# Optimization experiments

Hardware: AMD Instinct MI355X
Metric: run time of the kernel (lower is better)

The kernel has to match this reference:

```python
import jax, jax.numpy as jnp
import numpy as np

NUM_HEADS = 8
WIN = 8

def setup_inputs() -> dict:
    key = jax.random.key(0)
    k1, k2, k3 = jax.random.split(key, 3)
    B, H, W, C = 4, 256, 256, 256
    x = jax.random.normal(k1, (B, H, W, C), dtype=jnp.float32)
    w_qkv = jax.random.normal(k2, (C, 3 * C), dtype=jnp.float32) * (1.0 / np.sqrt(C))
    b_qkv = jnp.zeros((3 * C,), dtype=jnp.float32)
    w_proj = jax.random.normal(k3, (C, C), dtype=jnp.float32) * (1.0 / np.sqrt(C))
    b_proj = jnp.zeros((C,), dtype=jnp.float32)
    return {"x": x, "w_qkv": w_qkv, "b_qkv": b_qkv, "w_proj": w_proj, "b_proj": b_proj}

def reference(x, w_qkv, b_qkv, w_proj, b_proj):
    B, H, W, C = x.shape
    ws = WIN
    pad_h = (ws - H % ws) % ws
    pad_w = (ws - W % ws) % ws
    if pad_h > 0 or pad_w > 0:
        x = jnp.pad(x, ((0, 0), (0, pad_h), (0, pad_w), (0, 0)), mode='reflect')
        H, W = H + pad_h, W + pad_w
    Ho, Wo = H - pad_h, W - pad_w
    # window partition: [B, H//ws, ws, W//ws, ws, C] -> [nW, ws*ws, C]
    xw = x.reshape(B, H // ws, ws, W // ws, ws, C)
    xw = xw.transpose(0, 1, 3, 2, 4, 5).reshape(-1, ws * ws, C)
    head_dim = C // NUM_HEADS
    scale = head_dim ** (-0.5)
    qkv = xw @ w_qkv + b_qkv  # [nW, T, 3C]
    qkv = qkv.reshape(-1, ws * ws, 3, NUM_HEADS, head_dim).transpose(2, 0, 3, 1, 4)
    q, k, v = qkv[0], qkv[1], qkv[2]  # each [nW, h, T, d]
    attn = jnp.einsum('whtd,whsd->whts', q, k) * scale
    attn = jax.nn.softmax(attn, axis=-1)
    o = jnp.einsum('whts,whsd->whtd', attn, v)
    o = o.transpose(0, 2, 1, 3).reshape(-1, ws * ws, C)
    o = o @ w_proj + b_proj
    # window merge
    o = o.reshape(B, H // ws, W // ws, ws, ws, C)
    o = o.transpose(0, 1, 3, 2, 4, 5).reshape(B, H, W, C)
    return o[:, :Ho, :Wo, :]
```

## Files before the change

### kernel.cpp

```cpp
#include <hip/hip_runtime.h>
#include <hip/hip_bf16.h>

typedef __attribute__((ext_vector_type(8))) short short8;
typedef __attribute__((ext_vector_type(4))) short short4v;
typedef __attribute__((ext_vector_type(4))) float f32x4;

#define MFMA(a, b, c) __builtin_amdgcn_mfma_f32_16x16x32_bf16(a, b, c, 0, 0, 0)
#define XS(t, c) (((t) << 8) + ((c) ^ (((t) & 7) << 3)))

__device__ __forceinline__ unsigned int pk2(float lo, float hi) {
    union { __hip_bfloat162 h2; unsigned int u; } cv;
    cv.h2 = __float22bfloat162_rn(make_float2(lo, hi));
    return cv.u;
}

__device__ __forceinline__ unsigned short f2bf1(float f) {
    unsigned int u = __float_as_uint(f);
    u += 0x7FFFu + ((u >> 16) & 1u);
    return (unsigned short)(u >> 16);
}

__device__ __forceinline__ short4v u2s4(uint2 p) {
    union { uint2 u; short4v s; } t; t.u = p; return t.s;
}

#if __has_builtin(__builtin_amdgcn_mfma_f32_16x16x16bf16_1k)
__device__ __forceinline__ f32x4 mfma16(uint2 a, uint2 b, f32x4 c) {
    return __builtin_amdgcn_mfma_f32_16x16x16bf16_1k(u2s4(a), u2s4(b), c, 0, 0, 0);
}
#else
__device__ __forceinline__ short8 zfrag(uint2 p) {
    union { unsigned int u[4]; short8 s; } t;
    t.u[0] = p.x; t.u[1] = p.y; t.u[2] = 0u; t.u[3] = 0u;
    return t.s;
}
__device__ __forceinline__ f32x4 mfma16(uint2 a, uint2 b, f32x4 c) {
    return MFMA(zfrag(a), zfrag(b), c);
}
#endif

#define EXP2(x) exp2f(x)

__global__ void prep_w(const float* __restrict__ wqkv, const float* __restrict__ wproj,
                       unsigned short* __restrict__ wT) {
    int idx = blockIdx.x * 256 + threadIdx.x;
    if (idx < 196608) {
        const int frag   = idx >> 9;
        const int within = idx & 511;
        const int lane = within >> 3, j = within & 7;
        const int ks = frag & 7;
        const int dt = (frag >> 3) & 1;
        const int hh = (frag >> 4) & 7;
        const int m  = frag >> 7;
        const int n = m * 256 + hh * 32 + dt * 16 + (lane & 15);
        const int k = ks * 32 + ((lane >> 4) << 3) + j;
        wT[idx] = f2bf1(wqkv[k * 768 + n]);
    } else {
        const int r = idx - 196608;
        const int n = r >> 8, k = r & 255;
        wT[idx] = f2bf1(wproj[(k << 8) + n]);
    }
}

__global__ __launch_bounds__(256, 2)
void attn_qkv(const float* __restrict__ x,
              const float* __restrict__ bqkv,
              const unsigned short* __restrict__ wpk,
              unsigned short* __restrict__ Ob)
{
    __shared__ unsigned short smem[64 * 256];

    const int tid  = threadIdx.x;
    const int wid  = tid >> 6;
    const int lane = tid & 63;
    const int g    = lane >> 4;
    const int q16  = lane & 15;

    const int bid  = blockIdx.x;
    const int xcd  = bid & 7;
    const int q    = bid >> 3;
    const int widx = xcd * 512 + (q >> 1);
    const int hq   = (q & 1) << 2;
    const int h    = hq + wid;

    const int b  = widx >> 10;
    const int wh = (widx >> 5) & 31;
    const int ww = widx & 31;

    {
        const int t  = tid >> 2;
        const int c0 = (tid & 3) << 3;
        const int hr = (wh << 3) + (t >> 3);
        const int wc = (ww << 3) + (t & 7);
        const float* rowp = x + (((size_t)b * 256 + hr) * 256 + wc) * 256;
        #pragma unroll
        for (int u = 0; u < 8; ++u) {
            const int c = c0 + (u << 5);
            const float4 f0 = *reinterpret_cast<const float4*>(rowp + c);
            const float4 f1 = *reinterpret_cast<const float4*>(rowp + c + 4);
            union { unsigned int u4[4]; short8 s; } pv;
            pv.u4[0] = pk2(f0.x, f0.y); pv.u4[1] = pk2(f0.z, f0.w);
            pv.u4[2] = pk2(f1.x, f1.y); pv.u4[3] = pk2(f1.z, f1.w);
            *reinterpret_cast<short8*>(&smem[XS(t, c)]) = pv.s;
        }
    }
    __syncthreads();

    const f32x4 fz = {0.f, 0.f, 0.f, 0.f};
    const float SCL = 0.17677669529663687f * 1.4426950408889634f;
    const unsigned short* wh0 = wpk + ((size_t)h << 13);
    const int loff = lane << 3;

    uint2 pq[2][4];
    {
        f32x4 acc[2][4];
        #pragma unroll
        for (int dt = 0; dt < 2; ++dt)
            #pragma unroll
            for (int tt = 0; tt < 4; ++tt) acc[dt][tt] = fz;
        #pragma unroll
        for (int ks = 0; ks < 8; ++ks) {
            const int kc = ks << 5;
            short8 xf[4];
            #pragma unroll
            for (int tt = 0; tt < 4; ++tt)
                xf[tt] = *reinterpret_cast<const short8*>(&smem[XS(tt * 16 + q16, kc + (g << 3))]);
            #pragma unroll
            for (int dt = 0; dt < 2; ++dt) {
                const short8 wf = *reinterpret_cast<const short8*>(
                    wh0 + (((dt << 3) + ks) << 9) + loff);
                #pragma unroll
                for (int tt = 0; tt < 4; ++tt)
                    acc[dt][tt] = MFMA(wf, xf[tt], acc[dt][tt]);
            }
        }
        #pragma unroll
        for (int dt = 0; dt < 2; ++dt) {
            const float4 bb = *reinterpret_cast<const float4*>(bqkv + h * 32 + dt * 16 + (g << 2));
            #pragma unroll
            for (int tt = 0; tt < 4; ++tt) {
                const f32x4 a = acc[dt][tt];
                pq[dt][tt] = make_uint2(pk2((a[0] + bb.x) * SCL, (a[1] + bb.y) * SCL),
                                        pk2((a[2] + bb.z) * SCL, (a[3] + bb.w) * SCL));
            }
        }
    }

    uint2 pkk[2][4];
    {
        f32x4 acc[2][4];
        #pragma unroll
        for (int dt = 0; dt < 2; ++dt)
            #pragma unroll
            for (int tt = 0; tt < 4; ++tt) acc[dt][tt] = fz;
        const unsigned short* wb = wh0 + ((size_t)8 << 13);
        #pragma unroll
        for (int ks = 0; ks < 8; ++ks) {
            const int kc = ks << 5;
            short8 xf[4];
            #pragma unroll
            for (int tt = 0; tt < 4; ++tt)
                xf[tt] = *reinterpret_cast<const short8*>(&smem[XS(tt * 16 + q16, kc + (g << 3))]);
            #pragma unroll
            for (int dt = 0; dt < 2; ++dt) {
                const short8 wf = *reinterpret_cast<const short8*>(
                    wb + (((dt << 3) + ks) << 9) + loff);
                #pragma unroll
                for (int tt = 0; tt < 4; ++tt)
                    acc[dt][tt] = MFMA(wf, xf[tt], acc[dt][tt]);
            }
        }
        #pragma unroll
        for (int dt = 0; dt < 2; ++dt) {
            const float4 bb = *reinterpret_cast<const float4*>(bqkv + 256 + h * 32 + dt * 16 + (g << 2));
            #pragma unroll
            for (int tt = 0; tt < 4; ++tt) {
                const f32x4 a = acc[dt][tt];
                pkk[dt][tt] = make_uint2(pk2(a[0] + bb.x, a[1] + bb.y),
                                         pk2(a[2] + bb.z, a[3] + bb.w));
            }
        }
    }

    uint2 ppk[4][4];
    float inv4[4];
    #pragma unroll
    for (int qt = 0; qt < 4; ++qt) {
        f32x4 st[4];
        #pragma unroll
        for (int kt = 0; kt < 4; ++kt) st[kt] = fz;
        #pragma unroll
        for (int dt = 0; dt < 2; ++dt)
            #pragma unroll
            for (int kt = 0; kt < 4; ++kt)
                st[kt] = mfma16(pkk[dt][kt], pq[dt][qt], st[kt]);
        float sum = 0.f;
        #pragma unroll
        for (int kt = 0; kt < 4; ++kt) {
            const float e0 = EXP2(st[kt][0]), e1 = EXP2(st[kt][1]);
            const float e2 = EXP2(st[kt][2]), e3 = EXP2(st[kt][3]);
            sum += (e0 + e1) + (e2 + e3);
            ppk[kt][qt] = make_uint2(pk2(e0, e1), pk2(e2, e3));
        }
        sum += __shfl_xor(sum, 16);
        sum += __shfl_xor(sum, 32);
        inv4[qt] = 1.f / sum;
    }

    uint2 pv2[2][4];
    {
        f32x4 acc[2][4];
        #pragma unroll
        for (int dt = 0; dt < 2; ++dt)
            #pragma unroll
            for (int tt = 0; tt < 4; ++tt) acc[dt][tt] = fz;
        const unsigned short* wb = wh0 + ((size_t)16 << 13);
        #pragma unroll
        for (int ks = 0; ks < 8; ++ks) {
            const int kc = ks << 5;
            short8 xf[4];
            #pragma unroll
            for (int tt = 0; tt < 4; ++tt)
                xf[tt] = *reinterpret_cast<const short8*>(&smem[XS(tt * 16 + q16, kc + (g << 3))]);
            #pragma unroll
            for (int dt = 0; dt < 2; ++dt) {
                const short8 wf = *reinterpret_cast<const short8*>(
                    wb + (((dt << 3) + ks) << 9) + loff);
                #pragma unroll
                for (int tt = 0; tt < 4; ++tt)
                    acc[dt][tt] = MFMA(xf[tt], wf, acc[dt][tt]);
            }
        }
        #pragma unroll
        for (int dt = 0; dt < 2; ++dt) {
            const float bv = bqkv[512 + h * 32 + dt * 16 + q16];
            #pragma unroll
            for (int tt = 0; tt < 4; ++tt) {
                const f32x4 a = acc[dt][tt];
                pv2[dt][tt] = make_uint2(pk2(a[0] + bv, a[1] + bv),
                                         pk2(a[2] + bv, a[3] + bv));
            }
        }
    }

    f32x4 ot[2][4];
    #pragma unroll
    for (int dt = 0; dt < 2; ++dt)
        #pragma unroll
        for (int tt = 0; tt < 4; ++tt) ot[dt][tt] = fz;
    #pragma unroll
    for (int kt = 0; kt < 4; ++kt)
        #pragma unroll
        for (int tt = 0; tt < 4; ++tt)
            #pragma unroll
            for (int dt = 0; dt < 2; ++dt)
                ot[dt][tt] = mfma16(pv2[dt][kt], ppk[kt][tt], ot[dt][tt]);

    #pragma unroll
    for (int tt = 0; tt < 4; ++tt) {
        const float iv = inv4[tt];
        const int tok = tt * 16 + q16;
        const size_t srow = (((size_t)(b << 8) + (wh << 3) + (tok >> 3)) << 8)
                            + (ww << 3) + (tok & 7);
        unsigned short* drow = Ob + (srow << 8) + h * 32 + (g << 2);
        #pragma unroll
        for (int dt = 0; dt < 2; ++dt) {
            const uint2 pv = make_uint2(pk2(ot[dt][tt][0] * iv, ot[dt][tt][1] * iv),
                                        pk2(ot[dt][tt][2] * iv, ot[dt][tt][3] * iv));
            *reinterpret_cast<uint2*>(drow + dt * 16) = pv;
        }
    }
}

__global__ __launch_bounds__(256, 2)
void proj_gemm(const unsigned short* __restrict__ Ob,
               const unsigned short* __restrict__ wprojT,
               const float* __restrict__ bproj,
               float* __restrict__ out)
{
    __shared__ unsigned short As[2][128 * 64];
    __shared__ unsigned short Bs[2][128 * 64];

    const int tid  = threadIdx.x;
    const int wid  = tid >> 6;
    const int lane = tid & 63;
    const int g    = lane >> 4;
    const int q16  = lane & 15;
    const int wr   = wid >> 1, wc = wid & 1;

    const int bid = blockIdx.x;
    const int q   = bid >> 3;
    const int mt  = (bid & 7) * 256 + (q >> 1);
    const int nt  = q & 1;
    const size_t mrow0 = (size_t)mt << 7;
    const int nrow0 = nt << 7;

    const f32x4 fz = {0.f, 0.f, 0.f, 0.f};
    f32x4 acc[4][4];
    #pragma unroll
    for (int i = 0; i < 4; ++i)
        #pragma unroll
        for (int j = 0; j < 4; ++j) acc[i][j] = fz;

    int buf = 0;
    #pragma unroll
    for (int i = 0; i < 4; ++i) {
        const int chunk = (i << 8) + tid;
        const int r = chunk >> 3, c = chunk & 7;
        const int cs = c ^ (r & 7);
        const uint4 va = *reinterpret_cast<const uint4*>(Ob + ((mrow0 + r) << 8) + (c << 3));
        *reinterpret_cast<uint4*>(&As[0][(r << 6) + (cs << 3)]) = va;
        const uint4 vb = *reinterpret_cast<const uint4*>(wprojT + ((size_t)(nrow0 + r) << 8) + (c << 3));
        *reinterpret_cast<uint4*>(&Bs[0][(r << 6) + (cs << 3)]) = vb;
    }
    __syncthreads();

    for (int s = 0; s < 4; ++s) {
        if (s < 3) {
            const int so = (s + 1) << 6;
            #pragma unroll
            for (int i = 0; i < 4; ++i) {
                const int chunk = (i << 8) + tid;
                const int r = chunk >> 3, c = chunk & 7;
                const int cs = c ^ (r & 7);
                const uint4 va = *reinterpret_cast<const uint4*>(Ob + ((mrow0 + r) << 8) + so + (c << 3));
                *reinterpret_cast<uint4*>(&As[buf ^ 1][(r << 6) + (cs << 3)]) = va;
                const uint4 vb = *reinterpret_cast<const uint4*>(wprojT + ((size_t)(nrow0 + r) << 8) + so + (c << 3));
                *reinterpret_cast<uint4*>(&Bs[buf ^ 1][(r << 6) + (cs << 3)]) = vb;
            }
        }
        #pragma unroll
        for (int kk = 0; kk < 2; ++kk) {
            short8 aF[4], bF[4];
            #pragma unroll
            for (int i = 0; i < 4; ++i) {
                const int rA = (wr << 6) + (i << 4) + q16;
                const int cA = ((kk << 2) + g) ^ (rA & 7);
                aF[i] = *reinterpret_cast<const short8*>(&As[buf][(rA << 6) + (cA << 3)]);
                const int rB = (wc << 6) + (i << 4) + q16;
                const int cB = ((kk << 2) + g) ^ (rB & 7);
                bF[i] = *reinterpret_cast<const short8*>(&Bs[buf][(rB << 6) + (cB << 3)]);
            }
            #pragma unroll
            for (int i = 0; i < 4; ++i)
                #pragma unroll
                for (int j = 0; j < 4; ++j)
                    acc[i][j] = MFMA(aF[i], bF[j], acc[i][j]);
        }
        __syncthreads();
        buf ^= 1;
    }

    #pragma unroll
    for (int j = 0; j < 4; ++j) {
        const int coln = nrow0 + (wc << 6) + (j << 4) + q16;
        const float bp = bproj[coln];
        #pragma unroll
        for (int i = 0; i < 4; ++i) {
            const size_t row = mrow0 + (wr << 6) + (i << 4) + (g << 2);
            #pragma unroll
            for (int rr = 0; rr < 4; ++rr)
                out[((row + rr) << 8) + coln] = acc[i][j][rr] + bp;
        }
    }
}

extern "C" void kernel_launch(void* const* d_in, const int* in_sizes, int n_in,
                              void* d_out, int out_size, void* d_ws, size_t ws_size,
                              hipStream_t stream) {
    const float* x     = (const float*)d_in[0];
    const float* wqkv  = (const float*)d_in[1];
    const float* bqkv  = (const float*)d_in[2];
    const float* wproj = (const float*)d_in[3];
    const float* bproj = (const float*)d_in[4];
    float* out = (float*)d_out;
    unsigned short* wT = (unsigned short*)d_ws;

    prep_w<<<1024, 256, 0, stream>>>(wqkv, wproj, wT);
    unsigned short* Ob = wT + 262144;
    attn_qkv<<<8192, 256, 0, stream>>>(x, bqkv, wT, Ob);
    proj_gemm<<<4096, 256, 0, stream>>>(Ob, wT + 196608, bproj, out);
}
```

Measured before the change: 326.0 us.

## Process all heads per window block and stream Q per query tile

Each block now handles one window with a two-iteration loop over head groups, instead of two blocks each loading the same window for four heads. This halves the grid and removes the duplicated global load and bf16 conversion of x into shared memory. Q is now computed per 16-token query tile and fused with scores, softmax and PV, which lowers live register state. In exchange there are fewer blocks in flight and more sequential work per block, and W_q fragments are reloaded once per query tile.

```diff
diff --git a/kernel.cpp b/kernel.cpp
--- a/kernel.cpp
+++ b/kernel.cpp
@@ -77,11 +77,7 @@
     const int q16  = lane & 15;
 
     const int bid  = blockIdx.x;
-    const int xcd  = bid & 7;
-    const int q    = bid >> 3;
-    const int widx = xcd * 512 + (q >> 1);
-    const int hq   = (q & 1) << 2;
-    const int h    = hq + wid;
+    const int widx = (bid & 7) * 512 + (bid >> 3);
 
     const int b  = widx >> 10;
     const int wh = (widx >> 5) & 31;
@@ -108,166 +104,147 @@
 
     const f32x4 fz = {0.f, 0.f, 0.f, 0.f};
     const float SCL = 0.17677669529663687f * 1.4426950408889634f;
-    const unsigned short* wh0 = wpk + ((size_t)h << 13);
     const int loff = lane << 3;
 
-    uint2 pq[2][4];
-    {
-        f32x4 acc[2][4];
-        #pragma unroll
-        for (int dt = 0; dt < 2; ++dt)
-            #pragma unroll
-            for (int tt = 0; tt < 4; ++tt) acc[dt][tt] = fz;
-        #pragma unroll
-        for (int ks = 0; ks < 8; ++ks) {
-            const int kc = ks << 5;
-            short8 xf[4];
-            #pragma unroll
-            for (int tt = 0; tt < 4; ++tt)
-                xf[tt] = *reinterpret_cast<const short8*>(&smem[XS(tt * 16 + q16, kc + (g << 3))]);
+    for (int p = 0; p < 2; ++p) {
+        const int h = (p << 2) + wid;
+        const unsigned short* wh0 = wpk + ((size_t)h << 13);
+
+        uint2 pkk[2][4];
+        {
+            f32x4 acc[2][4];
+            #pragma unroll
+            for (int dt = 0; dt < 2; ++dt)
+                #pragma unroll
+                for (int tt = 0; tt < 4; ++tt) acc[dt][tt] = fz;
+            const unsigned short* wb = wh0 + ((size_t)8 << 13);
+            #pragma unroll
+            for (int ks = 0; ks < 8; ++ks) {
+                const int kc = ks << 5;
+                short8 xf[4];
+                #pragma unroll
+                for (int tt = 0; tt < 4; ++tt)
+                    xf[tt] = *reinterpret_cast<const short8*>(&smem[XS(tt * 16 + q16, kc + (g << 3))]);
+                #pragma unroll
+                for (int dt = 0; dt < 2; ++dt) {
+                    const short8 wf = *reinterpret_cast<const short8*>(
+                        wb + (((dt << 3) + ks) << 9) + loff);
+                    #pragma unroll
+                    for (int tt = 0; tt < 4; ++tt)
+                        acc[dt][tt] = MFMA(wf, xf[tt], acc[dt][tt]);
+                }
+            }
             #pragma unroll
             for (int dt = 0; dt < 2; ++dt) {
-                const short8 wf = *reinterpret_cast<const short8*>(
-                    wh0 + (((dt << 3) + ks) << 9) + loff);
+                const float4 bb = *reinterpret_cast<const float4*>(
+                    bqkv + 256 + h * 32 + dt * 16 + (g << 2));
+                #pragma unroll
+                for (int tt = 0; tt < 4; ++tt) {
+                    const f32x4 a = acc[dt][tt];
+                    pkk[dt][tt] = make_uint2(pk2(a[0] + bb.x, a[1] + bb.y),
+                                             pk2(a[2] + bb.z, a[3] + bb.w));
+                }
+            }
+        }
+
+        uint2 pv2[2][4];
+        {
+            f32x4 acc[2][4];
+            #pragma unroll
+            for (int dt = 0; dt < 2; ++dt)
+                #pragma unroll
+                for (int tt = 0; tt < 4; ++tt) acc[dt][tt] = fz;
+            const unsigned short* wb = wh0 + ((size_t)16 << 13);
+            #pragma unroll
+            for (int ks = 0; ks < 8; ++ks) {
+                const int kc = ks << 5;
+                short8 xf[4];
                 #pragma unroll
                 for (int tt = 0; tt < 4; ++tt)
-                    acc[dt][tt] = MFMA(wf, xf[tt], acc[dt][tt]);
-            }
-        }
-        #pragma unroll
-        for (int dt = 0; dt < 2; ++dt) {
-            const float4 bb = *reinterpret_cast<const float4*>(bqkv + h * 32 + dt * 16 + (g << 2));
-            #pragma unroll
-            for (int tt = 0; tt < 4; ++tt) {
-                const f32x4 a = acc[dt][tt];
-                pq[dt][tt] = make_uint2(pk2((a[0] + bb.x) * SCL, (a[1] + bb.y) * SCL),
-                                        pk2((a[2] + bb.z) * SCL, (a[3] + bb.w) * SCL));
-            }
-        }
-    }
-
-    uint2 pkk[2][4];
-    {
-        f32x4 acc[2][4];
-        #pragma unroll
-        for (int dt = 0; dt < 2; ++dt)
-            #pragma unroll
-            for (int tt = 0; tt < 4; ++tt) acc[dt][tt] = fz;
-        const unsigned short* wb = wh0 + ((size_t)8 << 13);
-        #pragma unroll
-        for (int ks = 0; ks < 8; ++ks) {
-            const int kc = ks << 5;
-            short8 xf[4];
-            #pragma unroll
-            for (int tt = 0; tt < 4; ++tt)
-                xf[tt] = *reinterpret_cast<const short8*>(&smem[XS(tt * 16 + q16, kc + (g << 3))]);
+                    xf[tt] = *reinterpret_cast<const short8*>(&smem[XS(tt * 16 + q16, kc + (g << 3))]);
+                #pragma unroll
+                for (int dt = 0; dt < 2; ++dt) {
+                    const short8 wf = *reinterpret_cast<const short8*>(
+                        wb + (((dt << 3) + ks) << 9) + loff);
+                    #pragma unroll
+                    for (int tt = 0; tt < 4; ++tt)
+                        acc[dt][tt] = MFMA(xf[tt], wf, acc[dt][tt]);
+                }
+            }
             #pragma unroll
             for (int dt = 0; dt < 2; ++dt) {
-                const short8 wf = *reinterpret_cast<const short8*>(
-                    wb + (((dt << 3) + ks) << 9) + loff);
-                #pragma unroll
-                for (int tt = 0; tt < 4; ++tt)
-                    acc[dt][tt] = MFMA(wf, xf[tt], acc[dt][tt]);
-            }
-        }
-        #pragma unroll
-        for (int dt = 0; dt < 2; ++dt) {
-            const float4 bb = *reinterpret_cast<const float4*>(bqkv + 256 + h * 32 + dt * 16 + (g << 2));
-            #pragma unroll
-            for (int tt = 0; tt < 4; ++tt) {
-                const f32x4 a = acc[dt][tt];
-                pkk[dt][tt] = make_uint2(pk2(a[0] + bb.x, a[1] + bb.y),
-                                         pk2(a[2] + bb.z, a[3] + bb.w));
-            }
-        }
-    }
-
-    uint2 ppk[4][4];
-    float inv4[4];
-    #pragma unroll
-    for (int qt = 0; qt < 4; ++qt) {
-        f32x4 st[4];
-        #pragma unroll
-        for (int kt = 0; kt < 4; ++kt) st[kt] = fz;
-        #pragma unroll
-        for (int dt = 0; dt < 2; ++dt)
+                const float bv = bqkv[512 + h * 32 + dt * 16 + q16];
+                #pragma unroll
+                for (int tt = 0; tt < 4; ++tt) {
+                    const f32x4 a = acc[dt][tt];
+                    pv2[dt][tt] = make_uint2(pk2(a[0] + bv, a[1] + bv),
+                                             pk2(a[2] + bv, a[3] + bv));
+                }
+            }
+        }
+
+        const float4 bbq0 = *reinterpret_cast<const float4*>(bqkv + h * 32 + (g << 2));
+        const float4 bbq1 = *reinterpret_cast<const float4*>(bqkv + h * 32 + 16 + (g << 2));
+        #pragma unroll
+        for (int qt = 0; qt < 4; ++qt) {
+            f32x4 accq[2] = {fz, fz};
+            #pragma unroll
+            for (int ks = 0; ks < 8; ++ks) {
+                const int kc = ks << 5;
+                const short8 xf = *reinterpret_cast<const short8*>(
+                    &smem[XS(qt * 16 + q16, kc + (g << 3))]);
+                #pragma unroll
+                for (int dt = 0; dt < 2; ++dt) {
+                    const short8 wf = *reinterpret_cast<const short8*>(
+                        wh0 + (((dt << 3) + ks) << 9) + loff);
+                    accq[dt] = MFMA(wf, xf, accq[dt]);
+                }
+            }
+            uint2 pqc[2];
+            pqc[0] = make_uint2(pk2((accq[0][0] + bbq0.x) * SCL, (accq[0][1] + bbq0.y) * SCL),
+                                pk2((accq[0][2] + bbq0.z) * SCL, (accq[0][3] + bbq0.w) * SCL));
+            pqc[1] = make_uint2(pk2((accq[1][0] + bbq1.x) * SCL, (accq[1][1] + bbq1.y) * SCL),
+                                pk2((accq[1][2] + bbq1.z) * SCL, (accq[1][3] + bbq1.w) * SCL));
+
+            f32x4 st[4];
+            #pragma unroll
+            for (int kt = 0; kt < 4; ++kt) st[kt] = fz;
+            #pragma unroll
+            for (int dt = 0; dt < 2; ++dt)
+                #pragma unroll
+                for (int kt = 0; kt < 4; ++kt)
+                    st[kt] = mfma16(pkk[dt][kt], pqc[dt], st[kt]);
+
+            uint2 ppkc[4];
+            float sum = 0.f;
+            #pragma unroll
+            for (int kt = 0; kt < 4; ++kt) {
+                const float e0 = EXP2(st[kt][0]), e1 = EXP2(st[kt][1]);
+                const float e2 = EXP2(st[kt][2]), e3 = EXP2(st[kt][3]);
+                sum += (e0 + e1) + (e2 + e3);
+                ppkc[kt] = make_uint2(pk2(e0, e1), pk2(e2, e3));
+            }
+            sum += __shfl_xor(sum, 16);
+            sum += __shfl_xor(sum, 32);
+            const float iv = 1.f / sum;
+
+            f32x4 otc[2] = {fz, fz};
             #pragma unroll
             for (int kt = 0; kt < 4; ++kt)
-                st[kt] = mfma16(pkk[dt][kt], pq[dt][qt], st[kt]);
-        float sum = 0.f;
-        #pragma unroll
-        for (int kt = 0; kt < 4; ++kt) {
-            const float e0 = EXP2(st[kt][0]), e1 = EXP2(st[kt][1]);
-            const float e2 = EXP2(st[kt][2]), e3 = EXP2(st[kt][3]);
-            sum += (e0 + e1) + (e2 + e3);
-            ppk[kt][qt] = make_uint2(pk2(e0, e1), pk2(e2, e3));
-        }
-        sum += __shfl_xor(sum, 16);
-        sum += __shfl_xor(sum, 32);
-        inv4[qt] = 1.f / sum;
-    }
-
-    uint2 pv2[2][4];
-    {
-        f32x4 acc[2][4];
-        #pragma unroll
-        for (int dt = 0; dt < 2; ++dt)
-            #pragma unroll
-            for (int tt = 0; tt < 4; ++tt) acc[dt][tt] = fz;
-        const unsigned short* wb = wh0 + ((size_t)16 << 13);
-        #pragma unroll
-        for (int ks = 0; ks < 8; ++ks) {
-            const int kc = ks << 5;
-            short8 xf[4];
-            #pragma unroll
-            for (int tt = 0; tt < 4; ++tt)
-                xf[tt] = *reinterpret_cast<const short8*>(&smem[XS(tt * 16 + q16, kc + (g << 3))]);
+                #pragma unroll
+                for (int dt = 0; dt < 2; ++dt)
+                    otc[dt] = mfma16(pv2[dt][kt], ppkc[kt], otc[dt]);
+
+            const int tok = qt * 16 + q16;
+            const size_t srow = (((size_t)(b << 8) + (wh << 3) + (tok >> 3)) << 8)
+                                + (ww << 3) + (tok & 7);
+            unsigned short* drow = Ob + (srow << 8) + h * 32 + (g << 2);
             #pragma unroll
             for (int dt = 0; dt < 2; ++dt) {
-                const short8 wf = *reinterpret_cast<const short8*>(
-                    wb + (((dt << 3) + ks) << 9) + loff);
-                #pragma unroll
-                for (int tt = 0; tt < 4; ++tt)
-                    acc[dt][tt] = MFMA(xf[tt], wf, acc[dt][tt]);
-            }
-        }
-        #pragma unroll
-        for (int dt = 0; dt < 2; ++dt) {
-            const float bv = bqkv[512 + h * 32 + dt * 16 + q16];
-            #pragma unroll
-            for (int tt = 0; tt < 4; ++tt) {
-                const f32x4 a = acc[dt][tt];
-                pv2[dt][tt] = make_uint2(pk2(a[0] + bv, a[1] + bv),
-                                         pk2(a[2] + bv, a[3] + bv));
-            }
-        }
-    }
-
-    f32x4 ot[2][4];
-    #pragma unroll
-    for (int dt = 0; dt < 2; ++dt)
-        #pragma unroll
-        for (int tt = 0; tt < 4; ++tt) ot[dt][tt] = fz;
-    #pragma unroll
-    for (int kt = 0; kt < 4; ++kt)
-        #pragma unroll
-        for (int tt = 0; tt < 4; ++tt)
-            #pragma unroll
-            for (int dt = 0; dt < 2; ++dt)
-                ot[dt][tt] = mfma16(pv2[dt][kt], ppk[kt][tt], ot[dt][tt]);
-
-    #pragma unroll
-    for (int tt = 0; tt < 4; ++tt) {
-        const float iv = inv4[tt];
-        const int tok = tt * 16 + q16;
-        const size_t srow = (((size_t)(b << 8) + (wh << 3) + (tok >> 3)) << 8)
-                            + (ww << 3) + (tok & 7);
-        unsigned short* drow = Ob + (srow << 8) + h * 32 + (g << 2);
-        #pragma unroll
-        for (int dt = 0; dt < 2; ++dt) {
-            const uint2 pv = make_uint2(pk2(ot[dt][tt][0] * iv, ot[dt][tt][1] * iv),
-                                        pk2(ot[dt][tt][2] * iv, ot[dt][tt][3] * iv));
-            *reinterpret_cast<uint2*>(drow + dt * 16) = pv;
+                const uint2 pv = make_uint2(pk2(otc[dt][0] * iv, otc[dt][1] * iv),
+                                            pk2(otc[dt][2] * iv, otc[dt][3] * iv));
+                *reinterpret_cast<uint2*>(drow + dt * 16) = pv;
+            }
         }
     }
 }
@@ -378,6 +355,6 @@
 
     prep_w<<<1024, 256, 0, stream>>>(wqkv, wproj, wT);
     unsigned short* Ob = wT + 262144;
-    attn_qkv<<<8192, 256, 0, stream>>>(x, bqkv, wT, Ob);
+    attn_qkv<<<4096, 256, 0, stream>>>(x, bqkv, wT, Ob);
     proj_gemm<<<4096, 256, 0, stream>>>(Ob, wT + 196608, bproj, out);
 }
```

New measurement: 471.6 us. 1.45x slower.

## Fuse Q, K, V projections into one pass over two token halves

Applied to the files above, without the earlier changes.

Merges the three separate Q, K and V projection loops into one loop that runs twice, once per half of the 64 window tokens, computing all three matrices for 32 tokens at a time. Each shared-memory x fragment is now loaded once for all three projections instead of three times, so LDS reads drop. In exchange, each of the 24 weight fragments per ks step is loaded twice (once per half) instead of once. Register pressure rises because pq, pkk and pv2 are all live before the scores are computed, and V is now computed before the softmax rather than after it.

```diff
diff --git a/kernel.cpp b/kernel.cpp
--- a/kernel.cpp
+++ b/kernel.cpp
@@ -111,73 +111,55 @@
     const unsigned short* wh0 = wpk + ((size_t)h << 13);
     const int loff = lane << 3;
 
-    uint2 pq[2][4];
-    {
-        f32x4 acc[2][4];
-        #pragma unroll
-        for (int dt = 0; dt < 2; ++dt)
-            #pragma unroll
-            for (int tt = 0; tt < 4; ++tt) acc[dt][tt] = fz;
+    uint2 pq[2][4], pkk[2][4], pv2[2][4];
+    #pragma unroll
+    for (int half = 0; half < 2; ++half) {
+        f32x4 acc[3][2][2];
+        #pragma unroll
+        for (int m = 0; m < 3; ++m)
+            #pragma unroll
+            for (int dt = 0; dt < 2; ++dt)
+                #pragma unroll
+                for (int t2 = 0; t2 < 2; ++t2) acc[m][dt][t2] = fz;
+
         #pragma unroll
         for (int ks = 0; ks < 8; ++ks) {
             const int kc = ks << 5;
-            short8 xf[4];
-            #pragma unroll
-            for (int tt = 0; tt < 4; ++tt)
-                xf[tt] = *reinterpret_cast<const short8*>(&smem[XS(tt * 16 + q16, kc + (g << 3))]);
-            #pragma unroll
-            for (int dt = 0; dt < 2; ++dt) {
-                const short8 wf = *reinterpret_cast<const short8*>(
-                    wh0 + (((dt << 3) + ks) << 9) + loff);
+            short8 xf[2];
+            #pragma unroll
+            for (int t2 = 0; t2 < 2; ++t2)
+                xf[t2] = *reinterpret_cast<const short8*>(
+                    &smem[XS(((half << 1) + t2) * 16 + q16, kc + (g << 3))]);
+            #pragma unroll
+            for (int m = 0; m < 3; ++m) {
                 #pragma unroll
-                for (int tt = 0; tt < 4; ++tt)
-                    acc[dt][tt] = MFMA(wf, xf[tt], acc[dt][tt]);
+                for (int dt = 0; dt < 2; ++dt) {
+                    const short8 wf = *reinterpret_cast<const short8*>(
+                        wh0 + (((size_t)m << 16) | (((dt << 3) + ks) << 9)) + loff);
+                    #pragma unroll
+                    for (int t2 = 0; t2 < 2; ++t2)
+                        acc[m][dt][t2] = (m < 2) ? MFMA(wf, xf[t2], acc[m][dt][t2])
+                                                 : MFMA(xf[t2], wf, acc[m][dt][t2]);
+                }
             }
         }
         #pragma unroll
         for (int dt = 0; dt < 2; ++dt) {
-            const float4 bb = *reinterpret_cast<const float4*>(bqkv + h * 32 + dt * 16 + (g << 2));
-            #pragma unroll
-            for (int tt = 0; tt < 4; ++tt) {
-                const f32x4 a = acc[dt][tt];
-                pq[dt][tt] = make_uint2(pk2((a[0] + bb.x) * SCL, (a[1] + bb.y) * SCL),
-                                        pk2((a[2] + bb.z) * SCL, (a[3] + bb.w) * SCL));
-            }
-        }
-    }
-
-    uint2 pkk[2][4];
-    {
-        f32x4 acc[2][4];
-        #pragma unroll
-        for (int dt = 0; dt < 2; ++dt)
-            #pragma unroll
-            for (int tt = 0; tt < 4; ++tt) acc[dt][tt] = fz;
-        const unsigned short* wb = wh0 + ((size_t)8 << 13);
-        #pragma unroll
-        for (int ks = 0; ks < 8; ++ks) {
-            const int kc = ks << 5;
-            short8 xf[4];
-            #pragma unroll
-            for (int tt = 0; tt < 4; ++tt)
-                xf[tt] = *reinterpret_cast<const short8*>(&smem[XS(tt * 16 + q16, kc + (g << 3))]);
-            #pragma unroll
-            for (int dt = 0; dt < 2; ++dt) {
-                const short8 wf = *reinterpret_cast<const short8*>(
-                    wb + (((dt << 3) + ks) << 9) + loff);
-                #pragma unroll
-                for (int tt = 0; tt < 4; ++tt)
-                    acc[dt][tt] = MFMA(wf, xf[tt], acc[dt][tt]);
-            }
-        }
-        #pragma unroll
-        for (int dt = 0; dt < 2; ++dt) {
-            const float4 bb = *reinterpret_cast<const float4*>(bqkv + 256 + h * 32 + dt * 16 + (g << 2));
-            #pragma unroll
-            for (int tt = 0; tt < 4; ++tt) {
-                const f32x4 a = acc[dt][tt];
-                pkk[dt][tt] = make_uint2(pk2(a[0] + bb.x, a[1] + bb.y),
-                                         pk2(a[2] + bb.z, a[3] + bb.w));
+            const float4 bbq = *reinterpret_cast<const float4*>(bqkv + h * 32 + dt * 16 + (g << 2));
+            const float4 bbk = *reinterpret_cast<const float4*>(bqkv + 256 + h * 32 + dt * 16 + (g << 2));
+            const float bv = bqkv[512 + h * 32 + dt * 16 + q16];
+            #pragma unroll
+            for (int t2 = 0; t2 < 2; ++t2) {
+                const int tt = (half << 1) + t2;
+                const f32x4 aq = acc[0][dt][t2];
+                pq[dt][tt]  = make_uint2(pk2((aq[0] + bbq.x) * SCL, (aq[1] + bbq.y) * SCL),
+                                         pk2((aq[2] + bbq.z) * SCL, (aq[3] + bbq.w) * SCL));
+                const f32x4 ak = acc[1][dt][t2];
+                pkk[dt][tt] = make_uint2(pk2(ak[0] + bbk.x, ak[1] + bbk.y),
+                                         pk2(ak[2] + bbk.z, ak[3] + bbk.w));
+                const f32x4 av = acc[2][dt][t2];
+                pv2[dt][tt] = make_uint2(pk2(av[0] + bv, av[1] + bv),
+                                         pk2(av[2] + bv, av[3] + bv));
             }
         }
     }
@@ -205,42 +187,6 @@
         sum += __shfl_xor(sum, 16);
         sum += __shfl_xor(sum, 32);
         inv4[qt] = 1.f / sum;
-    }
-
-    uint2 pv2[2][4];
-    {
-        f32x4 acc[2][4];
-        #pragma unroll
-        for (int dt = 0; dt < 2; ++dt)
-            #pragma unroll
-            for (int tt = 0; tt < 4; ++tt) acc[dt][tt] = fz;
-        const unsigned short* wb = wh0 + ((size_t)16 << 13);
-        #pragma unroll
-        for (int ks = 0; ks < 8; ++ks) {
-            const int kc = ks << 5;
-            short8 xf[4];
-            #pragma unroll
-            for (int tt = 0; tt < 4; ++tt)
-                xf[tt] = *reinterpret_cast<const short8*>(&smem[XS(tt * 16 + q16, kc + (g << 3))]);
-            #pragma unroll
-            for (int dt = 0; dt < 2; ++dt) {
-                const short8 wf = *reinterpret_cast<const short8*>(
-                    wb + (((dt << 3) + ks) << 9) + loff);
-                #pragma unroll
-                for (int tt = 0; tt < 4; ++tt)
-                    acc[dt][tt] = MFMA(xf[tt], wf, acc[dt][tt]);
-            }
-        }
-        #pragma unroll
-        for (int dt = 0; dt < 2; ++dt) {
-            const float bv = bqkv[512 + h * 32 + dt * 16 + q16];
-            #pragma unroll
-            for (int tt = 0; tt < 4; ++tt) {
-                const f32x4 a = acc[dt][tt];
-                pv2[dt][tt] = make_uint2(pk2(a[0] + bv, a[1] + bv),
-                                         pk2(a[2] + bv, a[3] + bv));
-            }
-        }
     }
 
     f32x4 ot[2][4];
```

New measurement: 309.6 us. 5.0% less time.
